# Performance work log

Measured on AMD Instinct MI355X. Metric: run time of the kernel, lower is better.

## Reference

```python
import jax, jax.numpy as jnp
import numpy as np

BI, BC = 128, 128      # image batch, caption batch
NR, NW = 36, 50        # regions per image, words per caption
EMB = 1024             # joint embedding dim
MASK = -1.0            # fill value for invalid (region, word) pairs


def setup_inputs() -> dict:
    key = jax.random.key(0)
    k1, k2, k3, k4 = jax.random.split(key, 4)
    imgs = jax.random.normal(k1, (BI, NR, EMB), dtype=jnp.float32)
    caps = jax.random.normal(k2, (BC, NW, EMB), dtype=jnp.float32)
    # valid lengths in [1, NR] / [1, NW]; force max so shapes are static
    img_lens = jax.random.randint(k3, (BI,), 1, NR + 1).at[0].set(NR).astype(jnp.int32)
    cap_lens = jax.random.randint(k4, (BC,), 1, NW + 1).at[0].set(NW).astype(jnp.int32)
    return {"imgs": imgs, "caps": caps, "img_lens": img_lens, "cap_lens": cap_lens}


def reference(imgs, caps, img_lens, cap_lens):
    # all-pairs region-word similarities: [bi, bc, n_r, n_w]
    n_r, n_w = imgs.shape[1], caps.shape[1]
    sims = jnp.einsum('ire,cwe->icrw', imgs, caps)
    # torch source computes sims under @torch.no_grad()
    sims = jax.lax.stop_gradient(sims)
    mask_i = jnp.arange(n_r) < img_lens[:, None]   # [bi, n_r]
    mask_c = jnp.arange(n_w) < cap_lens[:, None]   # [bc, n_w]
    mask = mask_i[:, None, :, None] & mask_c[None, :, None, :]  # [bi, bc, n_r, n_w]
    sims = jnp.where(mask, sims, MASK)
    # max-pool over region dim -> [bi, bc, n_w]
    return sims.max(axis=2)
```

## Files before the change

### kernel.cpp

```cpp
#include <hip/hip_runtime.h>
#include <cstdint>

#define NBI 128
#define NBC 128
#define NR_ 36
#define NW_ 50
#define EMB_ 1024
#define MTOT (NBI * NR_)
#define NTOT (NBC * NW_)
#define OUTN (NBI * NBC * NW_)

typedef _Float16 f16;
typedef _Float16 f16x8 __attribute__((ext_vector_type(8)));
typedef float f32x4 __attribute__((ext_vector_type(4)));

__device__ __forceinline__ uint32_t fkey(float v) {
  int32_t b = __float_as_int(v);
  return (b >= 0) ? ((uint32_t)b | 0x80000000u) : ~(uint32_t)b;
}

__global__ void zero_kernel(uint4* __restrict__ p, int n4) {
  int i = blockIdx.x * 256 + threadIdx.x;
  if (i < n4) p[i] = uint4{0u, 0u, 0u, 0u};
}

__global__ void cvt_kernel(const float* __restrict__ srcA, f16* __restrict__ dstA, int nA8,
                           const float* __restrict__ srcB, f16* __restrict__ dstB, int nB8) {
  int i = blockIdx.x * 256 + threadIdx.x;
  const float* src;
  f16* dst;
  if (i < nA8) {
    src = srcA; dst = dstA;
  } else {
    i -= nA8;
    if (i >= nB8) return;
    src = srcB; dst = dstB;
  }
  const float4* s = (const float4*)src;
  float4 a = s[2 * i];
  float4 b = s[2 * i + 1];
  union { f16 h[8]; uint4 u; } r;
  r.h[0] = (f16)a.x; r.h[1] = (f16)a.y; r.h[2] = (f16)a.z; r.h[3] = (f16)a.w;
  r.h[4] = (f16)b.x; r.h[5] = (f16)b.y; r.h[6] = (f16)b.z; r.h[7] = (f16)b.w;
  ((uint4*)dst)[i] = r.u;
}

__launch_bounds__(256, 3)
__global__ void gemm_max_kernel(const f16* __restrict__ A, const f16* __restrict__ B,
                                const int* __restrict__ img_lens,
                                uint32_t* __restrict__ mono) {
  __shared__ unsigned char smem[32768];

  const int bx = blockIdx.x;
  const int L = (bx & 7) * 225 + (bx >> 3);
  const int sc = L / 360;
  const int rem = L - sc * 360;
  const int bm = rem % 36;
  const int bn = sc * 10 + rem / 36;

  const int t = threadIdx.x;
  const int lane = t & 63;
  const int wv = t >> 6;
  const int wr = wv >> 1;
  const int wc = wv & 1;

  f32x4 acc[4][4] = {};

  const char* Ab = (const char*)A + (size_t)(bm * 128) * 2048;
  const char* Bb = (const char*)B + (size_t)(bn * 128) * 2048;

  int sdst[4];
  int sgof[4];
#pragma unroll
  for (int j = 0; j < 4; ++j) {
    int u = t + 256 * j;
    int row = u >> 3;
    int phys = (u & 7) * 16;
    int logical = phys ^ ((row & 7) << 4);
    sdst[j] = u * 16;
    sgof[j] = row * 2048 + logical;
  }

  for (int ck = 0; ck < 16; ++ck) {
    const int k0b = ck * 128;
#pragma unroll
    for (int j = 0; j < 4; ++j) {
      __builtin_amdgcn_global_load_lds(
          (const __attribute__((address_space(1))) void*)(Ab + (size_t)sgof[j] + k0b),
          (__attribute__((address_space(3))) void*)(smem + sdst[j]), 16, 0, 0);
    }
#pragma unroll
    for (int j = 0; j < 4; ++j) {
      __builtin_amdgcn_global_load_lds(
          (const __attribute__((address_space(1))) void*)(Bb + (size_t)sgof[j] + k0b),
          (__attribute__((address_space(3))) void*)(smem + 16384 + sdst[j]), 16, 0, 0);
    }
    __syncthreads();

#pragma unroll
    for (int kk = 0; kk < 2; ++kk) {
      f16x8 af[4], bf[4];
#pragma unroll
      for (int mt = 0; mt < 4; ++mt) {
        int row = wr * 64 + mt * 16 + (lane & 15);
        int col = (kk * 64 + (lane >> 4) * 16) ^ ((row & 7) << 4);
        af[mt] = *(const f16x8*)(smem + row * 128 + col);
      }
#pragma unroll
      for (int nt = 0; nt < 4; ++nt) {
        int row = wc * 64 + nt * 16 + (lane & 15);
        int col = (kk * 64 + (lane >> 4) * 16) ^ ((row & 7) << 4);
        bf[nt] = *(const f16x8*)(smem + 16384 + row * 128 + col);
      }
#pragma unroll
      for (int mt = 0; mt < 4; ++mt)
#pragma unroll
        for (int nt = 0; nt < 4; ++nt)
          acc[mt][nt] = __builtin_amdgcn_mfma_f32_16x16x32_f16(af[mt], bf[nt], acc[mt][nt], 0, 0, 0);
    }
    __syncthreads();
  }

  const int g0 = bm * 128 + wr * 64;
  const int i_first = g0 / 36;
  const int i_last = (g0 + 63) / 36;

#pragma unroll
  for (int nt = 0; nt < 4; ++nt) {
    const int col_g = bn * 128 + wc * 64 + nt * 16 + (lane & 15);
    for (int tgt = i_first; tgt <= i_last; ++tgt) {
      const int len = img_lens[tgt];
      float v = -3.0e38f;
#pragma unroll
      for (int mt = 0; mt < 4; ++mt) {
#pragma unroll
        for (int r4 = 0; r4 < 4; ++r4) {
          int gr = g0 + mt * 16 + ((lane >> 4) << 2) + r4;
          int ii = gr / 36;
          int rr = gr - ii * 36;
          if (ii == tgt && rr < len) v = fmaxf(v, acc[mt][nt][r4]);
        }
      }
      v = fmaxf(v, __shfl_xor(v, 16));
      v = fmaxf(v, __shfl_xor(v, 32));
      if ((lane >> 4) == 0 && v > -2.9e38f) {
        atomicMax(&mono[(size_t)tgt * 6400 + col_g], fkey(v));
      }
    }
  }
}

__global__ void finalize_kernel(const uint32_t* __restrict__ mono,
                                const int* __restrict__ img_lens,
                                const int* __restrict__ cap_lens,
                                float* __restrict__ out) {
  int idx = blockIdx.x * 256 + threadIdx.x;
  if (idx >= OUTN) return;
  int i = idx / (NBC * NW_);
  int rem = idx - i * (NBC * NW_);
  int c = rem / NW_;
  int w = rem - c * NW_;
  uint32_t k = mono[idx];
  int32_t b = (k & 0x80000000u) ? (int32_t)(k & 0x7FFFFFFFu) : (int32_t)~k;
  float v = __int_as_float(b);
  if (img_lens[i] < NR_) v = fmaxf(v, -1.0f);
  if (w >= cap_lens[c]) v = -1.0f;
  out[idx] = v;
}

extern "C" void kernel_launch(void* const* d_in, const int* in_sizes, int n_in,
                              void* d_out, int out_size, void* d_ws, size_t ws_size,
                              hipStream_t stream) {
  const float* imgs = (const float*)d_in[0];
  const float* caps = (const float*)d_in[1];
  const int* img_lens = (const int*)d_in[2];
  const int* cap_lens = (const int*)d_in[3];
  float* out = (float*)d_out;

  char* ws = (char*)d_ws;
  f16* Af = (f16*)ws;
  f16* Bf = (f16*)(ws + (size_t)MTOT * EMB_ * 2);
  uint32_t* mono = (uint32_t*)(ws + (size_t)MTOT * EMB_ * 2 + (size_t)NTOT * EMB_ * 2);

  const int nA8 = MTOT * EMB_ / 8;
  const int nB8 = NTOT * EMB_ / 8;
  const int ncvt = nA8 + nB8;

  zero_kernel<<<(OUTN / 4 + 255) / 256, 256, 0, stream>>>((uint4*)mono, OUTN / 4);
  cvt_kernel<<<(ncvt + 255) / 256, 256, 0, stream>>>(imgs, Af, nA8, caps, Bf, nB8);
  gemm_max_kernel<<<36 * 50, 256, 0, stream>>>(Af, Bf, img_lens, mono);
  finalize_kernel<<<(OUTN + 255) / 256, 256, 0, stream>>>(mono, img_lens, cap_lens, out);
}
```

Baseline: 168.4 us.

## Align GEMM M-tiles to image boundaries and fuse max-pool epilogue with direct output

The M tile grows from 128 to 144 rows (exactly four images of 36 regions), so each block owns whole images and can finish the region max-pool itself. The epilogue applies the masks and writes the final floats directly. This removes the zero-fill kernel, the atomicMax traffic through a monotonic-key buffer, and the finalize kernel. Each wave now computes a 144x32 slice (9x2 MFMA tiles) instead of 64x64. That raises A-fragment LDS reads per MFMA and register pressure, and the grid drops to 1600 blocks.

New measurement: 152.4 us. 9.5% less time.

```diff
diff --git a/kernel.cpp b/kernel.cpp
--- a/kernel.cpp
+++ b/kernel.cpp
@@ -8,21 +8,10 @@
 #define EMB_ 1024
 #define MTOT (NBI * NR_)
 #define NTOT (NBC * NW_)
-#define OUTN (NBI * NBC * NW_)
 
 typedef _Float16 f16;
 typedef _Float16 f16x8 __attribute__((ext_vector_type(8)));
 typedef float f32x4 __attribute__((ext_vector_type(4)));
-
-__device__ __forceinline__ uint32_t fkey(float v) {
-  int32_t b = __float_as_int(v);
-  return (b >= 0) ? ((uint32_t)b | 0x80000000u) : ~(uint32_t)b;
-}
-
-__global__ void zero_kernel(uint4* __restrict__ p, int n4) {
-  int i = blockIdx.x * 256 + threadIdx.x;
-  if (i < n4) p[i] = uint4{0u, 0u, 0u, 0u};
-}
 
 __global__ void cvt_kernel(const float* __restrict__ srcA, f16* __restrict__ dstA, int nA8,
                            const float* __restrict__ srcB, f16* __restrict__ dstB, int nB8) {
@@ -48,37 +37,45 @@
 __launch_bounds__(256, 3)
 __global__ void gemm_max_kernel(const f16* __restrict__ A, const f16* __restrict__ B,
                                 const int* __restrict__ img_lens,
-                                uint32_t* __restrict__ mono) {
-  __shared__ unsigned char smem[32768];
+                                const int* __restrict__ cap_lens,
+                                float* __restrict__ out) {
+  __shared__ unsigned char smem[34816];
 
   const int bx = blockIdx.x;
-  const int L = (bx & 7) * 225 + (bx >> 3);
-  const int sc = L / 360;
-  const int rem = L - sc * 360;
-  const int bm = rem % 36;
-  const int bn = sc * 10 + rem / 36;
+  const int L = (bx & 7) * 200 + (bx >> 3);
+  const int sc = L / 320;
+  const int rem = L - sc * 320;
+  const int bm = rem & 31;
+  const int bn = sc * 10 + (rem >> 5);
 
   const int t = threadIdx.x;
   const int lane = t & 63;
   const int wv = t >> 6;
-  const int wr = wv >> 1;
-  const int wc = wv & 1;
 
-  f32x4 acc[4][4] = {};
+  f32x4 acc[9][2] = {};
 
-  const char* Ab = (const char*)A + (size_t)(bm * 128) * 2048;
+  const char* Ab = (const char*)A + (size_t)(bm * 144) * 2048;
   const char* Bb = (const char*)B + (size_t)(bn * 128) * 2048;
 
-  int sdst[4];
-  int sgof[4];
+  int sdstA[5], sgofA[5];
+#pragma unroll
+  for (int j = 0; j < 5; ++j) {
+    int u = t + 256 * j;
+    int row = u >> 3;
+    int phys = (u & 7) * 16;
+    int logical = phys ^ ((row & 7) << 4);
+    sdstA[j] = u * 16;
+    sgofA[j] = row * 2048 + logical;
+  }
+  int sdstB[4], sgofB[4];
 #pragma unroll
   for (int j = 0; j < 4; ++j) {
     int u = t + 256 * j;
     int row = u >> 3;
     int phys = (u & 7) * 16;
     int logical = phys ^ ((row & 7) << 4);
-    sdst[j] = u * 16;
-    sgof[j] = row * 2048 + logical;
+    sdstB[j] = 18432 + u * 16;
+    sgofB[j] = row * 2048 + logical;
   }
 
   for (int ck = 0; ck < 16; ++ck) {
@@ -86,86 +83,80 @@
 #pragma unroll
     for (int j = 0; j < 4; ++j) {
       __builtin_amdgcn_global_load_lds(
-          (const __attribute__((address_space(1))) void*)(Ab + (size_t)sgof[j] + k0b),
-          (__attribute__((address_space(3))) void*)(smem + sdst[j]), 16, 0, 0);
+          (const __attribute__((address_space(1))) void*)(Ab + (size_t)sgofA[j] + k0b),
+          (__attribute__((address_space(3))) void*)(smem + sdstA[j]), 16, 0, 0);
+    }
+    if (t < 128) {
+      __builtin_amdgcn_global_load_lds(
+          (const __attribute__((address_space(1))) void*)(Ab + (size_t)sgofA[4] + k0b),
+          (__attribute__((address_space(3))) void*)(smem + sdstA[4]), 16, 0, 0);
     }
 #pragma unroll
     for (int j = 0; j < 4; ++j) {
       __builtin_amdgcn_global_load_lds(
-          (const __attribute__((address_space(1))) void*)(Bb + (size_t)sgof[j] + k0b),
-          (__attribute__((address_space(3))) void*)(smem + 16384 + sdst[j]), 16, 0, 0);
+          (const __attribute__((address_space(1))) void*)(Bb + (size_t)sgofB[j] + k0b),
+          (__attribute__((address_space(3))) void*)(smem + sdstB[j]), 16, 0, 0);
     }
     __syncthreads();
 
 #pragma unroll
     for (int kk = 0; kk < 2; ++kk) {
-      f16x8 af[4], bf[4];
+      f16x8 af[9], bf[2];
 #pragma unroll
-      for (int mt = 0; mt < 4; ++mt) {
-        int row = wr * 64 + mt * 16 + (lane & 15);
+      for (int mt = 0; mt < 9; ++mt) {
+        int row = mt * 16 + (lane & 15);
         int col = (kk * 64 + (lane >> 4) * 16) ^ ((row & 7) << 4);
         af[mt] = *(const f16x8*)(smem + row * 128 + col);
       }
 #pragma unroll
-      for (int nt = 0; nt < 4; ++nt) {
-        int row = wc * 64 + nt * 16 + (lane & 15);
+      for (int nt = 0; nt < 2; ++nt) {
+        int row = wv * 32 + nt * 16 + (lane & 15);
         int col = (kk * 64 + (lane >> 4) * 16) ^ ((row & 7) << 4);
-        bf[nt] = *(const f16x8*)(smem + 16384 + row * 128 + col);
+        bf[nt] = *(const f16x8*)(smem + 18432 + row * 128 + col);
       }
 #pragma unroll
-      for (int mt = 0; mt < 4; ++mt)
+      for (int mt = 0; mt < 9; ++mt)
 #pragma unroll
-        for (int nt = 0; nt < 4; ++nt)
+        for (int nt = 0; nt < 2; ++nt)
           acc[mt][nt] = __builtin_amdgcn_mfma_f32_16x16x32_f16(af[mt], bf[nt], acc[mt][nt], 0, 0, 0);
     }
     __syncthreads();
   }
 
-  const int g0 = bm * 128 + wr * 64;
-  const int i_first = g0 / 36;
-  const int i_last = (g0 + 63) / 36;
+  const int q4 = ((lane >> 4) << 2);
+  const int cg0 = bn * 128 + wv * 32 + (lane & 15);
+  const int cg1 = cg0 + 16;
+  const int c0 = cg0 / 50, w0 = cg0 - 50 * c0;
+  const int c1 = cg1 / 50, w1 = cg1 - 50 * c1;
+  const int cap0 = cap_lens[c0], cap1 = cap_lens[c1];
 
 #pragma unroll
-  for (int nt = 0; nt < 4; ++nt) {
-    const int col_g = bn * 128 + wc * 64 + nt * 16 + (lane & 15);
-    for (int tgt = i_first; tgt <= i_last; ++tgt) {
-      const int len = img_lens[tgt];
-      float v = -3.0e38f;
+  for (int k = 0; k < 4; ++k) {
+    const int gi = bm * 4 + k;
+    const int len = img_lens[gi];
+    const int lo = 36 * k, hi = 36 * k + len;
+    float v0 = -3.0e38f, v1 = -3.0e38f;
 #pragma unroll
-      for (int mt = 0; mt < 4; ++mt) {
+    for (int mt = 0; mt < 9; ++mt) {
 #pragma unroll
-        for (int r4 = 0; r4 < 4; ++r4) {
-          int gr = g0 + mt * 16 + ((lane >> 4) << 2) + r4;
-          int ii = gr / 36;
-          int rr = gr - ii * 36;
-          if (ii == tgt && rr < len) v = fmaxf(v, acc[mt][nt][r4]);
+      for (int r4 = 0; r4 < 4; ++r4) {
+        int row = mt * 16 + q4 + r4;
+        if (row >= lo && row < hi) {
+          v0 = fmaxf(v0, acc[mt][0][r4]);
+          v1 = fmaxf(v1, acc[mt][1][r4]);
         }
       }
-      v = fmaxf(v, __shfl_xor(v, 16));
-      v = fmaxf(v, __shfl_xor(v, 32));
-      if ((lane >> 4) == 0 && v > -2.9e38f) {
-        atomicMax(&mono[(size_t)tgt * 6400 + col_g], fkey(v));
-      }
+    }
+    v0 = fmaxf(v0, __shfl_xor(v0, 16)); v0 = fmaxf(v0, __shfl_xor(v0, 32));
+    v1 = fmaxf(v1, __shfl_xor(v1, 16)); v1 = fmaxf(v1, __shfl_xor(v1, 32));
+    if (len < NR_) { v0 = fmaxf(v0, -1.0f); v1 = fmaxf(v1, -1.0f); }
+    if (lane < 16) {
+      float o0 = (w0 >= cap0) ? -1.0f : v0;
+      float o1 = (w1 >= cap1) ? -1.0f : v1;
+      out[(size_t)gi * 6400 + cg0] = o0;
+      out[(size_t)gi * 6400 + cg1] = o1;
     }
   }
-}
-
-__global__ void finalize_kernel(const uint32_t* __restrict__ mono,
-                                const int* __restrict__ img_lens,
-                                const int* __restrict__ cap_lens,
-                                float* __restrict__ out) {
-  int idx = blockIdx.x * 256 + threadIdx.x;
-  if (idx >= OUTN) return;
-  int i = idx / (NBC * NW_);
-  int rem = idx - i * (NBC * NW_);
-  int c = rem / NW_;
-  int w = rem - c * NW_;
-  uint32_t k = mono[idx];
-  int32_t b = (k & 0x80000000u) ? (int32_t)(k & 0x7FFFFFFFu) : (int32_t)~k;
-  float v = __int_as_float(b);
-  if (img_lens[i] < NR_) v = fmaxf(v, -1.0f);
-  if (w >= cap_lens[c]) v = -1.0f;
-  out[idx] = v;
 }
 
 extern "C" void kernel_launch(void* const* d_in, const int* in_sizes, int n_in,
@@ -180,14 +171,11 @@
   char* ws = (char*)d_ws;
   f16* Af = (f16*)ws;
   f16* Bf = (f16*)(ws + (size_t)MTOT * EMB_ * 2);
-  uint32_t* mono = (uint32_t*)(ws + (size_t)MTOT * EMB_ * 2 + (size_t)NTOT * EMB_ * 2);
 
   const int nA8 = MTOT * EMB_ / 8;
   const int nB8 = NTOT * EMB_ / 8;
   const int ncvt = nA8 + nB8;
 
-  zero_kernel<<<(OUTN / 4 + 255) / 256, 256, 0, stream>>>((uint4*)mono, OUTN / 4);
   cvt_kernel<<<(ncvt + 255) / 256, 256, 0, stream>>>(imgs, Af, nA8, caps, Bf, nB8);
-  gemm_max_kernel<<<36 * 50, 256, 0, stream>>>(Af, Bf, img_lens, mono);
-  finalize_kernel<<<(OUTN + 255) / 256, 256, 0, stream>>>(mono, img_lens, cap_lens, out);
+  gemm_max_kernel<<<32 * 50, 256, 0, stream>>>(Af, Bf, img_lens, cap_lens, out);
 }
```
